# Kernel tuning notes

Measured on AMD Instinct MI355X. Metric: run time of the kernel, lower is better.

The kernel has to match this reference:

```python
import jax, jax.numpy as jnp
import numpy as np

B, P, ENC, DEC, EMB, ATT, V, L = 32, 196, 2048, 512, 512, 512, 32000, 21
T = L - 1  # decode steps


def setup_inputs() -> dict:
    key = jax.random.key(0)
    ks = jax.random.split(key, 20)
    u = lambda k, s, a=0.1: jax.random.uniform(k, s, jnp.float32, -a, a)
    lens = jax.random.randint(ks[1], (B, 1), 5, L + 1)
    lens = lens.at[0, 0].set(L)  # force max_decode_len == T (static)
    return {
        'encoder_out': jax.random.normal(ks[0], (B, P, ENC), jnp.float32),
        'encoded_captions': jax.random.randint(ks[2], (B, L), 0, V),
        'caption_lengths': lens,
        'emb_W': u(ks[3], (V, EMB)),
        'W_ea': u(ks[4], (ATT, ENC), 0.02), 'b_ea': jnp.zeros((ATT,)),
        'W_da': u(ks[5], (ATT, DEC), 0.02), 'b_da': jnp.zeros((ATT,)),
        'w_fa': u(ks[6], (1, ATT), 0.02), 'b_fa': jnp.zeros((1,)),
        'W_ih': u(ks[7], (4 * DEC, EMB + ENC), 0.02), 'b_ih': jnp.zeros((4 * DEC,)),
        'W_hh': u(ks[8], (4 * DEC, DEC), 0.02), 'b_hh': jnp.zeros((4 * DEC,)),
        'W_h0': u(ks[9], (DEC, ENC), 0.02), 'b_h0': jnp.zeros((DEC,)),
        'W_c0': u(ks[10], (DEC, ENC), 0.02), 'b_c0': jnp.zeros((DEC,)),
        'W_fb': u(ks[11], (ENC, DEC), 0.02), 'b_fb': jnp.zeros((ENC,)),
        'W_fc': u(ks[12], (V, DEC)), 'b_fc': jnp.zeros((V,)),
    }


def reference(encoder_out, encoded_captions, caption_lengths, emb_W,
              W_ea, b_ea, W_da, b_da, w_fa, b_fa,
              W_ih, b_ih, W_hh, b_hh, W_h0, b_h0, W_c0, b_c0,
              W_fb, b_fb, W_fc, b_fc):
    # sort by caption length descending (as in torch forward)
    lens = caption_lengths[:, 0]
    sort_ind = jnp.argsort(-lens)
    lens_s = lens[sort_ind]
    enc = encoder_out[sort_ind]          # [B,P,ENC]
    caps = encoded_captions[sort_ind]    # [B,L]
    dec_lens = lens_s - 1

    mean_enc = enc.mean(axis=1)
    h0 = mean_enc @ W_h0.T + b_h0
    c0 = mean_enc @ W_c0.T + b_c0

    att1 = jnp.einsum('bpe,ae->bpa', enc, W_ea) + b_ea  # precompute encoder attn proj
    embs = emb_W[caps]                                   # [B,L,EMB]
    emb_seq = jnp.transpose(embs[:, :T], (1, 0, 2))      # [T,B,EMB] (teacher forcing)
    mask_seq = jnp.arange(T)[:, None] < dec_lens[None, :]  # [T,B]

    def step(carry, xs):
        h, c = carry
        emb_t, m = xs  # [B,EMB], [B] bool; m emulates shrinking batch_size_t
        att2 = h @ W_da.T + b_da
        e = jnp.maximum(att1 + att2[:, None, :], 0.0) @ w_fa[0] + b_fa[0]  # [B,P]
        alpha = jax.nn.softmax(e, axis=1)
        awe = jnp.einsum('bp,bpe->be', alpha, enc)
        gate = jax.nn.sigmoid(h @ W_fb.T + b_fb)
        x = jnp.concatenate([emb_t, gate * awe], axis=1)
        g = x @ W_ih.T + b_ih + h @ W_hh.T + b_hh
        i, f, gg, o = jnp.split(g, 4, axis=1)
        c_new = jax.nn.sigmoid(f) * c + jax.nn.sigmoid(i) * jnp.tanh(gg)
        h_new = jax.nn.sigmoid(o) * jnp.tanh(c_new)
        preds = h_new @ W_fc.T + b_fc  # dropout in eval mode (identity)
        mf = m[:, None]
        h = jnp.where(mf, h_new, h)
        c = jnp.where(mf, c_new, c)
        preds = preds * mf.astype(preds.dtype)
        alpha = alpha * mf.astype(alpha.dtype)
        return (h, c), (preds, alpha)

    _, (preds, alphas) = jax.lax.scan(step, (h0, c0), (emb_seq, mask_seq))
    predictions = jnp.transpose(preds, (1, 0, 2))  # [B,T,V]
    alphas = jnp.transpose(alphas, (1, 0, 2))      # [B,T,P]
    return predictions, alphas
```

## Files before the change

### kernel.cpp

```cpp
#include <hip/hip_runtime.h>
#include <hip/hip_bf16.h>
#include <cstddef>

#define NB 32
#define NP 196
#define NE 2048
#define ND 512
#define NV 32000
#define NL 21
#define NT 20

typedef __attribute__((ext_vector_type(8))) short short8;
typedef __attribute__((ext_vector_type(4))) float f32x4;

__device__ __forceinline__ unsigned short f2b(float f) {
    __hip_bfloat16 h = __float2bfloat16(f);
    return *reinterpret_cast<unsigned short*>(&h);
}
__device__ __forceinline__ float b2f(unsigned short u) {
    union { unsigned int i; float f; } v; v.i = (unsigned)u << 16; return v.f;
}
__device__ __forceinline__ float b2f_lo(unsigned int u) {
    union { unsigned int i; float f; } v; v.i = u << 16; return v.f;
}
__device__ __forceinline__ float b2f_hi(unsigned int u) {
    union { unsigned int i; float f; } v; v.i = u & 0xffff0000u; return v.f;
}


__global__ void k_sort(const int* __restrict__ lens, int* __restrict__ sind, int* __restrict__ dlens,
                       int* __restrict__ rowmap, int* __restrict__ mpad)
{
    int i = threadIdx.x;
    if (i < NB) {
        int li = lens[i];
        int r = 0;
        for (int j = 0; j < NB; ++j) {
            int lj = lens[j];
            if (lj > li || (lj == li && j < i)) ++r;
        }
        sind[r] = i;
        dlens[r] = li - 1;
    }
    __syncthreads();
    if (i == 0) {
        int c = 0;
        for (int t = 0; t < NT; ++t)
            for (int b = 0; b < NB; ++b)
                if (t < dlens[b]) rowmap[c++] = t * NB + b;
        int pad = (c + 63) & ~63;
        for (int r = c; r < pad; ++r) rowmap[r] = -1;
        mpad[0] = pad;
    }
}

__global__ __launch_bounds__(256) void k_conv_enc(
    const float* __restrict__ enc, const int* __restrict__ sind,
    unsigned short* __restrict__ encB)
{
    int idx = (blockIdx.x * 256 + threadIdx.x) * 8;
    int b = idx / (NP * NE), rem = idx - b * (NP * NE);
    const float* src = enc + (size_t)sind[b] * NP * NE + rem;
    float4 a = *reinterpret_cast<const float4*>(src);
    float4 c = *reinterpret_cast<const float4*>(src + 4);
    uint4 o;
    o.x = f2b(a.x) | ((unsigned)f2b(a.y) << 16);
    o.y = f2b(a.z) | ((unsigned)f2b(a.w) << 16);
    o.z = f2b(c.x) | ((unsigned)f2b(c.y) << 16);
    o.w = f2b(c.z) | ((unsigned)f2b(c.w) << 16);
    *reinterpret_cast<uint4*>(encB + idx) = o;
}

__global__ __launch_bounds__(256) void k_mean(const float* __restrict__ enc, const int* __restrict__ sind,
                                              float* __restrict__ mean_enc)
{
    int b = blockIdx.y;
    int k = blockIdx.x * 256 + threadIdx.x;
    const float* e = enc + (size_t)sind[b] * NP * NE + k;
    float s0 = 0.f, s1 = 0.f, s2 = 0.f, s3 = 0.f;
    for (int p = 0; p < NP; p += 4) {
        s0 += e[(size_t)(p + 0) * NE];
        s1 += e[(size_t)(p + 1) * NE];
        s2 += e[(size_t)(p + 2) * NE];
        s3 += e[(size_t)(p + 3) * NE];
    }
    mean_enc[(size_t)b * NE + k] = (s0 + s1 + s2 + s3) * (1.0f / NP);
}

__global__ __launch_bounds__(256) void k_zero(const int* __restrict__ dlens, float* __restrict__ out)
{
    int b = blockIdx.x / NT, t = blockIdx.x % NT;
    if (t < dlens[b]) return;
    float4 z = {0.f, 0.f, 0.f, 0.f};
    float4* row = (float4*)(out + ((size_t)b * NT + t) * NV);
    for (int i = threadIdx.x; i < NV / 4; i += 256) row[i] = z;
}

__global__ __launch_bounds__(256) void gemm_skinny_split(
    const float* __restrict__ A0, const float* __restrict__ W0a, const float* __restrict__ W0b,
    float* __restrict__ spart)
{
    __shared__ float As[32][32];
    __shared__ float Ws[64][33];
    int n0 = blockIdx.x * 64;
    int ks = blockIdx.y;
    int tid = threadIdx.x;
    int lb = tid / 8, lkq = tid % 8;
    int b4 = (tid / 32) * 4, nl = (tid % 32) * 2;
    float acc[4][2] = {};
    for (int kt = ks * 256; kt < ks * 256 + 256; kt += 32) {
        float4 a4 = *reinterpret_cast<const float4*>(A0 + (size_t)lb * NE + kt + lkq * 4);
        As[lkq * 4 + 0][lb] = a4.x; As[lkq * 4 + 1][lb] = a4.y;
        As[lkq * 4 + 2][lb] = a4.z; As[lkq * 4 + 3][lb] = a4.w;
        #pragma unroll
        for (int r = 0; r < 2; ++r) {
            int s = tid + r * 256;
            int n_l = s / 8, kq = s % 8;
            int ng = n0 + n_l;
            const float* wrow = (ng < 512) ? (W0a + (size_t)ng * NE)
                                           : (W0b + (size_t)(ng - 512) * NE);
            float4 w4 = *reinterpret_cast<const float4*>(wrow + kt + kq * 4);
            Ws[n_l][kq * 4 + 0] = w4.x; Ws[n_l][kq * 4 + 1] = w4.y;
            Ws[n_l][kq * 4 + 2] = w4.z; Ws[n_l][kq * 4 + 3] = w4.w;
        }
        __syncthreads();
        #pragma unroll
        for (int k = 0; k < 32; ++k) {
            float4 av = *reinterpret_cast<const float4*>(&As[k][b4]);
            float w0 = Ws[nl][k], w1 = Ws[nl + 1][k];
            acc[0][0] += av.x * w0; acc[0][1] += av.x * w1;
            acc[1][0] += av.y * w0; acc[1][1] += av.y * w1;
            acc[2][0] += av.z * w0; acc[2][1] += av.z * w1;
            acc[3][0] += av.w * w0; acc[3][1] += av.w * w1;
        }
        __syncthreads();
    }
    float* Cp = spart + (size_t)ks * NB * 1024;
    #pragma unroll
    for (int j = 0; j < 2; ++j)
        #pragma unroll
        for (int i = 0; i < 4; ++i)
            Cp[(size_t)(b4 + i) * 1024 + n0 + nl + j] = acc[i][j];
}

__global__ __launch_bounds__(256) void k_hc0(
    const float* __restrict__ spart, const float* __restrict__ ba, const float* __restrict__ bb,
    float* __restrict__ hc, float* __restrict__ xh)
{
    int b = blockIdx.x;
    for (int ng = threadIdx.x; ng < 1024; ng += 256) {
        float s = (ng < 512) ? ba[ng] : bb[ng - 512];
        #pragma unroll
        for (int ks = 0; ks < 8; ++ks)
            s += spart[(size_t)ks * NB * 1024 + (size_t)b * 1024 + ng];
        hc[(size_t)b * 1024 + ng] = s;
        if (ng < 512) xh[(size_t)b * 3072 + 2560 + ng] = s;
    }
}

__global__ __launch_bounds__(256) void gemm_att1_mfma(
    const unsigned short* __restrict__ encB, const float* __restrict__ W_ea,
    const float* __restrict__ bias, unsigned short* __restrict__ att1B)
{
    int fid = blockIdx.x;
    int c = fid & 7, x = (fid >> 3) & 7, pg = fid >> 6;
    int p = pg * 8 + c;
    if (p >= 98) return;
    int bm0 = p * 64, bn0 = x * 64;
    __shared__ unsigned short As[64][40];
    __shared__ unsigned short Bs[64][40];
    int tid = threadIdx.x;
    int w = tid >> 6, lane = tid & 63;
    int srow = tid >> 2, schunk = (tid & 3) * 8;
    const unsigned short* arow = encB + (size_t)(bm0 + srow) * NE + schunk;
    const float* brow = W_ea + (size_t)(bn0 + srow) * NE + schunk;
    int frow = lane & 15, fk = (lane >> 4) * 8;
    f32x4 acc[4] = {};
    for (int kt = 0; kt < NE; kt += 32) {
        uint4 av = *reinterpret_cast<const uint4*>(arow + kt);
        float4 b0 = *reinterpret_cast<const float4*>(brow + kt);
        float4 b1 = *reinterpret_cast<const float4*>(brow + kt + 4);
        uint4 bv;
        bv.x = f2b(b0.x) | ((unsigned)f2b(b0.y) << 16);
        bv.y = f2b(b0.z) | ((unsigned)f2b(b0.w) << 16);
        bv.z = f2b(b1.x) | ((unsigned)f2b(b1.y) << 16);
        bv.w = f2b(b1.z) | ((unsigned)f2b(b1.w) << 16);
        *reinterpret_cast<uint4*>(&As[srow][schunk]) = av;
        *reinterpret_cast<uint4*>(&Bs[srow][schunk]) = bv;
        __syncthreads();
        short8 af = *reinterpret_cast<const short8*>(&As[w * 16 + frow][fk]);
        #pragma unroll
        for (int n = 0; n < 4; ++n) {
            short8 bf = *reinterpret_cast<const short8*>(&Bs[n * 16 + frow][fk]);
            acc[n] = __builtin_amdgcn_mfma_f32_16x16x32_bf16(af, bf, acc[n], 0, 0, 0);
        }
        __syncthreads();
    }
    int crow = bm0 + w * 16 + (lane >> 4) * 4;
    int ccol0 = lane & 15;
    #pragma unroll
    for (int n = 0; n < 4; ++n) {
        int col = bn0 + n * 16 + ccol0;
        float bb2 = bias[col];
        #pragma unroll
        for (int i = 0; i < 4; ++i)
            att1B[(size_t)(crow + i) * ND + col] = f2b(acc[n][i] + bb2);
    }
}

__global__ __launch_bounds__(256) void gemm_preds_mfma(
    const unsigned short* __restrict__ hseqB, const float* __restrict__ W_fc,
    const float* __restrict__ bias, float* __restrict__ out,
    const int* __restrict__ rowmap, const int* __restrict__ mpad)
{
    int fid = blockIdx.x;
    int c = fid & 7;
    int rem = fid >> 3;
    int m = rem % 10, g = rem / 10;
    int n = g * 8 + c;
    if (n >= 250) return;
    int bm0 = m * 64;
    if (bm0 >= mpad[0]) return;
    int bn0 = n * 128;
    __shared__ unsigned short As[64][40];
    __shared__ unsigned short Bs[128][40];
    int tid = threadIdx.x;
    int w = tid >> 6, lane = tid & 63;
    int srow = tid >> 2, schunk = (tid & 3) * 8;
    int rid = rowmap[bm0 + srow];
    const unsigned short* aptr = hseqB + (size_t)(rid < 0 ? 0 : rid) * ND + schunk;
    const float* bptr0 = W_fc + (size_t)(bn0 + srow) * ND + schunk;
    const float* bptr1 = W_fc + (size_t)(bn0 + 64 + srow) * ND + schunk;
    int frow = lane & 15, fk = (lane >> 4) * 8;
    f32x4 acc[8] = {};
    for (int kt = 0; kt < ND; kt += 32) {
        uint4 av = *reinterpret_cast<const uint4*>(aptr + kt);
        float4 c0 = *reinterpret_cast<const float4*>(bptr0 + kt);
        float4 c1 = *reinterpret_cast<const float4*>(bptr0 + kt + 4);
        float4 d0 = *reinterpret_cast<const float4*>(bptr1 + kt);
        float4 d1 = *reinterpret_cast<const float4*>(bptr1 + kt + 4);
        uint4 bv0, bv1;
        bv0.x = f2b(c0.x) | ((unsigned)f2b(c0.y) << 16);
        bv0.y = f2b(c0.z) | ((unsigned)f2b(c0.w) << 16);
        bv0.z = f2b(c1.x) | ((unsigned)f2b(c1.y) << 16);
        bv0.w = f2b(c1.z) | ((unsigned)f2b(c1.w) << 16);
        bv1.x = f2b(d0.x) | ((unsigned)f2b(d0.y) << 16);
        bv1.y = f2b(d0.z) | ((unsigned)f2b(d0.w) << 16);
        bv1.z = f2b(d1.x) | ((unsigned)f2b(d1.y) << 16);
        bv1.w = f2b(d1.z) | ((unsigned)f2b(d1.w) << 16);
        *reinterpret_cast<uint4*>(&As[srow][schunk]) = av;
        *reinterpret_cast<uint4*>(&Bs[srow][schunk]) = bv0;
        *reinterpret_cast<uint4*>(&Bs[64 + srow][schunk]) = bv1;
        __syncthreads();
        short8 af = *reinterpret_cast<const short8*>(&As[w * 16 + frow][fk]);
        #pragma unroll
        for (int nn = 0; nn < 8; ++nn) {
            short8 bf = *reinterpret_cast<const short8*>(&Bs[nn * 16 + frow][fk]);
            acc[nn] = __builtin_amdgcn_mfma_f32_16x16x32_bf16(af, bf, acc[nn], 0, 0, 0);
        }
        __syncthreads();
    }
    int rl0 = w * 16 + (lane >> 4) * 4;
    int ccol0 = lane & 15;
    #pragma unroll
    for (int i = 0; i < 4; ++i) {
        int rm = rowmap[bm0 + rl0 + i];
        if (rm < 0) continue;
        int t = rm / NB, b = rm % NB;
        float* orow = out + ((size_t)b * NT + t) * NV;
        #pragma unroll
        for (int nn = 0; nn < 8; ++nn) {
            int col = bn0 + nn * 16 + ccol0;
            orow[col] = acc[nn][i] + bias[col];
        }
    }
}

__global__ __launch_bounds__(256) void k_attg(
    const float* __restrict__ hc, const float* __restrict__ W_da, const float* __restrict__ W_fb,
    const float* __restrict__ b_da, const float* __restrict__ b_fb, float* __restrict__ attg)
{
    __shared__ float As[32][32];
    __shared__ float Ws[64][33];
    int n0 = blockIdx.x * 64;
    int tid = threadIdx.x;
    int lb = tid / 8, lkq = tid % 8;
    int b4 = (tid / 32) * 4, nl = (tid % 32) * 2;
    float acc[4][2] = {};
    for (int kt = 0; kt < 512; kt += 32) {
        float4 a4 = *reinterpret_cast<const float4*>(hc + (size_t)lb * 1024 + kt + lkq * 4);
        As[lkq * 4 + 0][lb] = a4.x; As[lkq * 4 + 1][lb] = a4.y;
        As[lkq * 4 + 2][lb] = a4.z; As[lkq * 4 + 3][lb] = a4.w;
        #pragma unroll
        for (int r = 0; r < 2; ++r) {
            int s = tid + r * 256;
            int n_l = s / 8, kq = s % 8;
            int ng = n0 + n_l;
            const float* wrow = (ng < 512) ? (W_da + (size_t)ng * 512)
                                           : (W_fb + (size_t)(ng - 512) * 512);
            float4 w4 = *reinterpret_cast<const float4*>(wrow + kt + kq * 4);
            Ws[n_l][kq * 4 + 0] = w4.x; Ws[n_l][kq * 4 + 1] = w4.y;
            Ws[n_l][kq * 4 + 2] = w4.z; Ws[n_l][kq * 4 + 3] = w4.w;
        }
        __syncthreads();
        #pragma unroll
        for (int k = 0; k < 32; ++k) {
            float4 av = *reinterpret_cast<const float4*>(&As[k][b4]);
            float w0 = Ws[nl][k], w1 = Ws[nl + 1][k];
            acc[0][0] += av.x * w0; acc[0][1] += av.x * w1;
            acc[1][0] += av.y * w0; acc[1][1] += av.y * w1;
            acc[2][0] += av.z * w0; acc[2][1] += av.z * w1;
            acc[3][0] += av.w * w0; acc[3][1] += av.w * w1;
        }
        __syncthreads();
    }
    #pragma unroll
    for (int j = 0; j < 2; ++j) {
        int ng = n0 + nl + j;
        float bias = (ng < 512) ? b_da[ng] : b_fb[ng - 512];
        #pragma unroll
        for (int i = 0; i < 4; ++i)
            attg[(size_t)(b4 + i) * 2560 + ng] = acc[i][j] + bias;
    }
}

__global__ __launch_bounds__(256) void k_e(
    const unsigned short* __restrict__ att1B, const float* __restrict__ attg,
    const float* __restrict__ w_fa, const float* __restrict__ b_fa,
    float* __restrict__ e)
{
    __shared__ float att2s[ND];
    __shared__ float wfas[ND];
    int b = blockIdx.y, tid = threadIdx.x;
    const float* ag = attg + (size_t)b * 2560;
    for (int d = tid; d < ND; d += 256) { att2s[d] = ag[d]; wfas[d] = w_fa[d]; }
    __syncthreads();
    int w = tid >> 6, lane = tid & 63;
    int p0 = blockIdx.x * 28;
    const unsigned short* a1 = att1B + ((size_t)b * NP + p0) * ND;
    #pragma unroll
    for (int i = 0; i < 7; ++i) {
        int p = w + 4 * i;
        const unsigned short* row = a1 + (size_t)p * ND;
        float s = 0.f;
        #pragma unroll
        for (int j = 0; j < 2; ++j) {
            int d = j * 256 + lane * 4;
            uint2 u = *reinterpret_cast<const uint2*>(row + d);
            float v0 = b2f_lo(u.x), v1 = b2f_hi(u.x);
            float v2 = b2f_lo(u.y), v3 = b2f_hi(u.y);
            float4 a2 = *reinterpret_cast<const float4*>(&att2s[d]);
            float4 wf = *reinterpret_cast<const float4*>(&wfas[d]);
            s += fmaxf(v0 + a2.x, 0.f) * wf.x + fmaxf(v1 + a2.y, 0.f) * wf.y
               + fmaxf(v2 + a2.z, 0.f) * wf.z + fmaxf(v3 + a2.w, 0.f) * wf.w;
        }
        for (int off = 32; off > 0; off >>= 1) s += __shfl_down(s, off);
        if (lane == 0) e[(size_t)b * NP + p0 + p] = s + b_fa[0];
    }
}

__global__ __launch_bounds__(256) void k_awe(
    const unsigned short* __restrict__ encB, const int* __restrict__ dlens,
    const int* __restrict__ sind, const int* __restrict__ caps, const float* __restrict__ emb_W,
    const float* __restrict__ e, const float* __restrict__ attg,
    float* __restrict__ xh, float* __restrict__ out_alpha, int t)
{
    __shared__ float es[256];
    __shared__ float red[256];
    int kc = blockIdx.x, b = blockIdx.y, tid = threadIdx.x;
    float ev = -1e30f;
    if (tid < NP) { float v = e[(size_t)b * NP + tid]; es[tid] = v; ev = v; }
    red[tid] = ev; __syncthreads();
    for (int s2 = 128; s2 > 0; s2 >>= 1) { if (tid < s2) red[tid] = fmaxf(red[tid], red[tid + s2]); __syncthreads(); }
    float m = red[0]; __syncthreads();
    float xe = (tid < NP) ? expf(es[tid] - m) : 0.f;
    red[tid] = xe; __syncthreads();
    for (int s2 = 128; s2 > 0; s2 >>= 1) { if (tid < s2) red[tid] += red[tid + s2]; __syncthreads(); }
    float inv = 1.0f / red[0];
    __syncthreads();
    es[tid] = xe * inv;
    __syncthreads();

    int k = kc * 256 + tid;
    const unsigned short* ec = encB + (size_t)b * NP * NE + k;
    float s0 = 0.f, s1 = 0.f, s2v = 0.f, s3 = 0.f;
    #pragma unroll 4
    for (int p = 0; p < NP; p += 4) {
        s0 += es[p + 0] * b2f(ec[(size_t)(p + 0) * NE]);
        s1 += es[p + 1] * b2f(ec[(size_t)(p + 1) * NE]);
        s2v += es[p + 2] * b2f(ec[(size_t)(p + 2) * NE]);
        s3 += es[p + 3] * b2f(ec[(size_t)(p + 3) * NE]);
    }
    float awe = (s0 + s1) + (s2v + s3);
    float gp = attg[(size_t)b * 2560 + 512 + k];
    float gate = 1.f / (1.f + expf(-gp));
    xh[(size_t)b * 3072 + 512 + k] = gate * awe;
    if (kc == 0) {
        bool live = (t < dlens[b]);
        if (tid < NP) out_alpha[((size_t)b * NT + t) * NP + tid] = live ? es[tid] : 0.f;
        const float* er = emb_W + (size_t)caps[sind[b] * NL + t] * ND;
        xh[(size_t)b * 3072 + tid] = er[tid];
        xh[(size_t)b * 3072 + 256 + tid] = er[256 + tid];
    }
}

__global__ __launch_bounds__(256) void k_gates(
    const float* __restrict__ xh, const float* __restrict__ W_ih, const float* __restrict__ W_hh,
    float* __restrict__ gpart)
{
    __shared__ float smem[3200];
    int blk = blockIdx.x, tid = threadIdx.x;
    int nt = blk & 31, ks = blk >> 5;
    float* As = smem;
    float (*Ws)[33] = (float(*)[33])(smem + 1024);
    int n0 = nt * 64;
    int lb = tid / 8, lkq = tid % 8;
    int b4 = (tid / 32) * 4, nl = (tid % 32) * 2;
    float acc[4][2] = {};
    for (int kt = ks * 768; kt < ks * 768 + 768; kt += 32) {
        float4 a4 = *reinterpret_cast<const float4*>(xh + (size_t)lb * 3072 + kt + lkq * 4);
        As[(lkq * 4 + 0) * 32 + lb] = a4.x; As[(lkq * 4 + 1) * 32 + lb] = a4.y;
        As[(lkq * 4 + 2) * 32 + lb] = a4.z; As[(lkq * 4 + 3) * 32 + lb] = a4.w;
        #pragma unroll
        for (int r = 0; r < 2; ++r) {
            int s = tid + r * 256;
            int n_l = s / 8, kq = s % 8;
            int ng = n0 + n_l;
            int kk = kt + kq * 4;
            const float* wrow = (kk < 2560) ? (W_ih + (size_t)ng * 2560 + kk)
                                            : (W_hh + (size_t)ng * 512 + (kk - 2560));
            float4 w4 = *reinterpret_cast<const float4*>(wrow);
            Ws[n_l][kq * 4 + 0] = w4.x; Ws[n_l][kq * 4 + 1] = w4.y;
            Ws[n_l][kq * 4 + 2] = w4.z; Ws[n_l][kq * 4 + 3] = w4.w;
        }
        __syncthreads();
        #pragma unroll
        for (int k = 0; k < 32; ++k) {
            float4 av = *reinterpret_cast<const float4*>(&As[k * 32 + b4]);
            float w0 = Ws[nl][k], w1 = Ws[nl + 1][k];
            acc[0][0] += av.x * w0; acc[0][1] += av.x * w1;
            acc[1][0] += av.y * w0; acc[1][1] += av.y * w1;
            acc[2][0] += av.z * w0; acc[2][1] += av.z * w1;
            acc[3][0] += av.w * w0; acc[3][1] += av.w * w1;
        }
        __syncthreads();
    }
    float* Cp = gpart + (size_t)ks * NB * 2048;
    #pragma unroll
    for (int j = 0; j < 2; ++j)
        #pragma unroll
        for (int i = 0; i < 4; ++i)
            Cp[(size_t)(b4 + i) * 2048 + n0 + nl + j] = acc[i][j];
}

__global__ __launch_bounds__(256) void k_cell(
    const float* __restrict__ gpart, const int* __restrict__ dlens,
    const float* __restrict__ b_ih, const float* __restrict__ b_hh,
    float* __restrict__ hc, unsigned short* __restrict__ hseqB, float* __restrict__ xh, int t)
{
    int b = blockIdx.x;
    for (int d = threadIdx.x; d < ND; d += 256) {
        float g0 = b_ih[d] + b_hh[d];
        float g1 = b_ih[512 + d] + b_hh[512 + d];
        float g2 = b_ih[1024 + d] + b_hh[1024 + d];
        float g3 = b_ih[1536 + d] + b_hh[1536 + d];
        #pragma unroll
        for (int ks = 0; ks < 4; ++ks) {
            const float* gp = gpart + ((size_t)ks * NB + b) * 2048;
            g0 += gp[d]; g1 += gp[512 + d]; g2 += gp[1024 + d]; g3 += gp[1536 + d];
        }
        float ig = 1.f / (1.f + expf(-g0));
        float fg = 1.f / (1.f + expf(-g1));
        float gt = tanhf(g2);
        float og = 1.f / (1.f + expf(-g3));
        float c_old = hc[(size_t)b * 1024 + 512 + d];
        float c_new = fg * c_old + ig * gt;
        float h_new = og * tanhf(c_new);
        hseqB[((size_t)t * NB + b) * ND + d] = f2b(h_new);
        if (t < dlens[b]) {
            hc[(size_t)b * 1024 + d] = h_new;
            hc[(size_t)b * 1024 + 512 + d] = c_new;
            xh[(size_t)b * 3072 + 2560 + d] = h_new;
        }
    }
}

extern "C" void kernel_launch(void* const* d_in, const int* in_sizes, int n_in,
                              void* d_out, int out_size, void* d_ws, size_t ws_size,
                              hipStream_t stream)
{
    const float* enc   = (const float*)d_in[0];
    const int*   caps  = (const int*)d_in[1];
    const int*   clens = (const int*)d_in[2];
    const float* emb_W = (const float*)d_in[3];
    const float* W_ea  = (const float*)d_in[4];
    const float* b_ea  = (const float*)d_in[5];
    const float* W_da  = (const float*)d_in[6];
    const float* b_da  = (const float*)d_in[7];
    const float* w_fa  = (const float*)d_in[8];
    const float* b_fa  = (const float*)d_in[9];
    const float* W_ih  = (const float*)d_in[10];
    const float* b_ih  = (const float*)d_in[11];
    const float* W_hh  = (const float*)d_in[12];
    const float* b_hh  = (const float*)d_in[13];
    const float* W_h0  = (const float*)d_in[14];
    const float* b_h0  = (const float*)d_in[15];
    const float* W_c0  = (const float*)d_in[16];
    const float* b_c0  = (const float*)d_in[17];
    const float* W_fb  = (const float*)d_in[18];
    const float* b_fb  = (const float*)d_in[19];
    const float* W_fc  = (const float*)d_in[20];
    const float* b_fc  = (const float*)d_in[21];

    float* out = (float*)d_out;
    float* out_alpha = out + (size_t)NB * NT * NV;

    int* iws    = (int*)d_ws;
    int* sind   = iws;
    int* dlens  = iws + 32;
    int* rowmap = iws + 64;
    int* mpad   = iws + 704;
    float* base = (float*)d_ws + 1024;
    float* mean_enc = base;
    float* hc    = mean_enc + NB * NE;
    float* attg  = hc + NB * 1024;
    float* xh    = attg + NB * 2560;
    float* e     = xh + NB * 3072;
    float* gpart = e + NB * NP;
    unsigned short* att1B = (unsigned short*)(gpart + 262144);
    unsigned short* hseqB = att1B + (size_t)NB * NP * ND;
    unsigned short* encB  = hseqB + (size_t)NT * NB * ND;

    k_sort<<<1, 64, 0, stream>>>(clens, sind, dlens, rowmap, mpad);
    k_zero<<<NB * NT, 256, 0, stream>>>(dlens, out);
    k_conv_enc<<<dim3(NB * NP * NE / 2048), 256, 0, stream>>>(enc, sind, encB);
    k_mean<<<dim3(NE / 256, NB), 256, 0, stream>>>(enc, sind, mean_enc);
    gemm_skinny_split<<<dim3(16, 8), 256, 0, stream>>>(mean_enc, W_h0, W_c0, gpart);
    k_hc0<<<dim3(NB), 256, 0, stream>>>(gpart, b_h0, b_c0, hc, xh);
    gemm_att1_mfma<<<dim3(832), 256, 0, stream>>>(encB, W_ea, b_ea, att1B);

    for (int t = 0; t < NT; ++t) {
        k_attg<<<dim3(40), 256, 0, stream>>>(hc, W_da, W_fb, b_da, b_fb, attg);
        k_e<<<dim3(7, NB), 256, 0, stream>>>(att1B, attg, w_fa, b_fa, e);
        k_awe<<<dim3(8, NB), 256, 0, stream>>>(encB, dlens, sind, caps, emb_W,
                                               e, attg, xh, out_alpha, t);
        k_gates<<<dim3(128), 256, 0, stream>>>(xh, W_ih, W_hh, gpart);
        k_cell<<<dim3(NB), 256, 0, stream>>>(gpart, dlens, b_ih, b_hh, hc, hseqB, xh, t);
    }

    gemm_preds_mfma<<<dim3(2560), 256, 0, stream>>>(hseqB, W_fc, b_fc, out, rowmap, mpad);
}
```

Before: 1.805 ms.

## Move embedding and recurrent gate GEMMs off the attention critical path

The embedding and W_hh parts of the LSTM gate GEMM are now computed in the first phase of each step, alongside the attention/gate projection, since they do not depend on the attention output. The post-attention gate kernel then only covers the 2048-wide attention-weighted encoding slice, which shortens the serial chain per step. Embeddings are gathered for all steps up front by a new kernel. The att1 GEMM now reads and converts fp32 encoder rows directly instead of the bf16 copy. The cell kernel sums six partial buffers instead of four.

Result: faster. 1.580 ms (median of 2 runs) (-12.5%).

```diff
diff --git a/kernel.cpp b/kernel.cpp
--- a/kernel.cpp
+++ b/kernel.cpp
@@ -71,6 +71,17 @@
     *reinterpret_cast<uint4*>(encB + idx) = o;
 }
 
+__global__ __launch_bounds__(256) void k_emb(
+    const int* __restrict__ caps, const int* __restrict__ sind,
+    const float* __restrict__ emb_W, float* __restrict__ embS)
+{
+    int t = blockIdx.x, b = blockIdx.y;
+    const float* src = emb_W + (size_t)caps[sind[b] * NL + t] * ND;
+    float* dst = embS + ((size_t)t * NB + b) * ND;
+    int i = threadIdx.x * 2;
+    *reinterpret_cast<float2*>(dst + i) = *reinterpret_cast<const float2*>(src + i);
+}
+
 __global__ __launch_bounds__(256) void k_mean(const float* __restrict__ enc, const int* __restrict__ sind,
                                               float* __restrict__ mean_enc)
 {
@@ -96,11 +107,44 @@
     for (int i = threadIdx.x; i < NV / 4; i += 256) row[i] = z;
 }
 
+__device__ __forceinline__ void tile_body_uniW(
+    const float* __restrict__ A, int lda, const float* __restrict__ W, int wstride,
+    int n0, int kbeg, int kend, float* As, float (*Ws)[33], float acc[4][2],
+    int tid)
+{
+    int lb = tid / 8, lkq = tid % 8;
+    int b4 = (tid / 32) * 4, nl = (tid % 32) * 2;
+    for (int kt = kbeg; kt < kend; kt += 32) {
+        float4 a4 = *reinterpret_cast<const float4*>(A + (size_t)lb * lda + kt + lkq * 4);
+        As[(lkq * 4 + 0) * 32 + lb] = a4.x; As[(lkq * 4 + 1) * 32 + lb] = a4.y;
+        As[(lkq * 4 + 2) * 32 + lb] = a4.z; As[(lkq * 4 + 3) * 32 + lb] = a4.w;
+        #pragma unroll
+        for (int r = 0; r < 2; ++r) {
+            int s = tid + r * 256;
+            int n_l = s / 8, kq = s % 8;
+            float4 w4 = *reinterpret_cast<const float4*>(W + (size_t)(n0 + n_l) * wstride + kt + kq * 4);
+            Ws[n_l][kq * 4 + 0] = w4.x; Ws[n_l][kq * 4 + 1] = w4.y;
+            Ws[n_l][kq * 4 + 2] = w4.z; Ws[n_l][kq * 4 + 3] = w4.w;
+        }
+        __syncthreads();
+        #pragma unroll
+        for (int k = 0; k < 32; ++k) {
+            float4 av = *reinterpret_cast<const float4*>(&As[k * 32 + b4]);
+            float w0 = Ws[nl][k], w1 = Ws[nl + 1][k];
+            acc[0][0] += av.x * w0; acc[0][1] += av.x * w1;
+            acc[1][0] += av.y * w0; acc[1][1] += av.y * w1;
+            acc[2][0] += av.z * w0; acc[2][1] += av.z * w1;
+            acc[3][0] += av.w * w0; acc[3][1] += av.w * w1;
+        }
+        __syncthreads();
+    }
+}
+
 __global__ __launch_bounds__(256) void gemm_skinny_split(
     const float* __restrict__ A0, const float* __restrict__ W0a, const float* __restrict__ W0b,
     float* __restrict__ spart)
 {
-    __shared__ float As[32][32];
+    __shared__ float As[1024];
     __shared__ float Ws[64][33];
     int n0 = blockIdx.x * 64;
     int ks = blockIdx.y;
@@ -110,8 +154,8 @@
     float acc[4][2] = {};
     for (int kt = ks * 256; kt < ks * 256 + 256; kt += 32) {
         float4 a4 = *reinterpret_cast<const float4*>(A0 + (size_t)lb * NE + kt + lkq * 4);
-        As[lkq * 4 + 0][lb] = a4.x; As[lkq * 4 + 1][lb] = a4.y;
-        As[lkq * 4 + 2][lb] = a4.z; As[lkq * 4 + 3][lb] = a4.w;
+        As[(lkq * 4 + 0) * 32 + lb] = a4.x; As[(lkq * 4 + 1) * 32 + lb] = a4.y;
+        As[(lkq * 4 + 2) * 32 + lb] = a4.z; As[(lkq * 4 + 3) * 32 + lb] = a4.w;
         #pragma unroll
         for (int r = 0; r < 2; ++r) {
             int s = tid + r * 256;
@@ -126,7 +170,7 @@
         __syncthreads();
         #pragma unroll
         for (int k = 0; k < 32; ++k) {
-            float4 av = *reinterpret_cast<const float4*>(&As[k][b4]);
+            float4 av = *reinterpret_cast<const float4*>(&As[k * 32 + b4]);
             float w0 = Ws[nl][k], w1 = Ws[nl + 1][k];
             acc[0][0] += av.x * w0; acc[0][1] += av.x * w1;
             acc[1][0] += av.y * w0; acc[1][1] += av.y * w1;
@@ -145,7 +189,7 @@
 
 __global__ __launch_bounds__(256) void k_hc0(
     const float* __restrict__ spart, const float* __restrict__ ba, const float* __restrict__ bb,
-    float* __restrict__ hc, float* __restrict__ xh)
+    float* __restrict__ hc)
 {
     int b = blockIdx.x;
     for (int ng = threadIdx.x; ng < 1024; ng += 256) {
@@ -154,13 +198,13 @@
         for (int ks = 0; ks < 8; ++ks)
             s += spart[(size_t)ks * NB * 1024 + (size_t)b * 1024 + ng];
         hc[(size_t)b * 1024 + ng] = s;
-        if (ng < 512) xh[(size_t)b * 3072 + 2560 + ng] = s;
     }
 }
 
 __global__ __launch_bounds__(256) void gemm_att1_mfma(
-    const unsigned short* __restrict__ encB, const float* __restrict__ W_ea,
-    const float* __restrict__ bias, unsigned short* __restrict__ att1B)
+    const float* __restrict__ enc, const float* __restrict__ W_ea,
+    const float* __restrict__ bias, unsigned short* __restrict__ att1B,
+    const int* __restrict__ sind)
 {
     int fid = blockIdx.x;
     int c = fid & 7, x = (fid >> 3) & 7, pg = fid >> 6;
@@ -172,15 +216,22 @@
     int tid = threadIdx.x;
     int w = tid >> 6, lane = tid & 63;
     int srow = tid >> 2, schunk = (tid & 3) * 8;
-    const unsigned short* arow = encB + (size_t)(bm0 + srow) * NE + schunk;
+    int mg = bm0 + srow;
+    int bidx = mg / NP, pp = mg - bidx * NP;
+    const float* arow = enc + ((size_t)sind[bidx] * NP + pp) * NE + schunk;
     const float* brow = W_ea + (size_t)(bn0 + srow) * NE + schunk;
     int frow = lane & 15, fk = (lane >> 4) * 8;
     f32x4 acc[4] = {};
     for (int kt = 0; kt < NE; kt += 32) {
-        uint4 av = *reinterpret_cast<const uint4*>(arow + kt);
+        float4 a0 = *reinterpret_cast<const float4*>(arow + kt);
+        float4 a1 = *reinterpret_cast<const float4*>(arow + kt + 4);
         float4 b0 = *reinterpret_cast<const float4*>(brow + kt);
         float4 b1 = *reinterpret_cast<const float4*>(brow + kt + 4);
-        uint4 bv;
+        uint4 av, bv;
+        av.x = f2b(a0.x) | ((unsigned)f2b(a0.y) << 16);
+        av.y = f2b(a0.z) | ((unsigned)f2b(a0.w) << 16);
+        av.z = f2b(a1.x) | ((unsigned)f2b(a1.y) << 16);
+        av.w = f2b(a1.z) | ((unsigned)f2b(a1.w) << 16);
         bv.x = f2b(b0.x) | ((unsigned)f2b(b0.y) << 16);
         bv.y = f2b(b0.z) | ((unsigned)f2b(b0.w) << 16);
         bv.z = f2b(b1.x) | ((unsigned)f2b(b1.y) << 16);
@@ -276,51 +327,73 @@
     }
 }
 
-__global__ __launch_bounds__(256) void k_attg(
+__global__ __launch_bounds__(256) void k_phase1(
     const float* __restrict__ hc, const float* __restrict__ W_da, const float* __restrict__ W_fb,
-    const float* __restrict__ b_da, const float* __restrict__ b_fb, float* __restrict__ attg)
-{
-    __shared__ float As[32][32];
+    const float* __restrict__ b_da, const float* __restrict__ b_fb,
+    const float* __restrict__ embS, const float* __restrict__ W_ih, const float* __restrict__ W_hh,
+    float* __restrict__ attg, float* __restrict__ gpart, int t)
+{
+    __shared__ float As[1024];
     __shared__ float Ws[64][33];
-    int n0 = blockIdx.x * 64;
-    int tid = threadIdx.x;
-    int lb = tid / 8, lkq = tid % 8;
+    int blk = blockIdx.x, tid = threadIdx.x;
     int b4 = (tid / 32) * 4, nl = (tid % 32) * 2;
     float acc[4][2] = {};
-    for (int kt = 0; kt < 512; kt += 32) {
-        float4 a4 = *reinterpret_cast<const float4*>(hc + (size_t)lb * 1024 + kt + lkq * 4);
-        As[lkq * 4 + 0][lb] = a4.x; As[lkq * 4 + 1][lb] = a4.y;
-        As[lkq * 4 + 2][lb] = a4.z; As[lkq * 4 + 3][lb] = a4.w;
-        #pragma unroll
-        for (int r = 0; r < 2; ++r) {
-            int s = tid + r * 256;
-            int n_l = s / 8, kq = s % 8;
-            int ng = n0 + n_l;
-            const float* wrow = (ng < 512) ? (W_da + (size_t)ng * 512)
-                                           : (W_fb + (size_t)(ng - 512) * 512);
-            float4 w4 = *reinterpret_cast<const float4*>(wrow + kt + kq * 4);
-            Ws[n_l][kq * 4 + 0] = w4.x; Ws[n_l][kq * 4 + 1] = w4.y;
-            Ws[n_l][kq * 4 + 2] = w4.z; Ws[n_l][kq * 4 + 3] = w4.w;
-        }
-        __syncthreads();
-        #pragma unroll
-        for (int k = 0; k < 32; ++k) {
-            float4 av = *reinterpret_cast<const float4*>(&As[k][b4]);
-            float w0 = Ws[nl][k], w1 = Ws[nl + 1][k];
-            acc[0][0] += av.x * w0; acc[0][1] += av.x * w1;
-            acc[1][0] += av.y * w0; acc[1][1] += av.y * w1;
-            acc[2][0] += av.z * w0; acc[2][1] += av.z * w1;
-            acc[3][0] += av.w * w0; acc[3][1] += av.w * w1;
-        }
-        __syncthreads();
-    }
-    #pragma unroll
-    for (int j = 0; j < 2; ++j) {
-        int ng = n0 + nl + j;
-        float bias = (ng < 512) ? b_da[ng] : b_fb[ng - 512];
-        #pragma unroll
-        for (int i = 0; i < 4; ++i)
-            attg[(size_t)(b4 + i) * 2560 + ng] = acc[i][j] + bias;
+    if (blk < 40) {
+        int n0 = blk * 64;
+        int lb = tid / 8, lkq = tid % 8;
+        for (int kt = 0; kt < 512; kt += 32) {
+            float4 a4 = *reinterpret_cast<const float4*>(hc + (size_t)lb * 1024 + kt + lkq * 4);
+            As[(lkq * 4 + 0) * 32 + lb] = a4.x; As[(lkq * 4 + 1) * 32 + lb] = a4.y;
+            As[(lkq * 4 + 2) * 32 + lb] = a4.z; As[(lkq * 4 + 3) * 32 + lb] = a4.w;
+            #pragma unroll
+            for (int r = 0; r < 2; ++r) {
+                int s = tid + r * 256;
+                int n_l = s / 8, kq = s % 8;
+                int ng = n0 + n_l;
+                const float* wrow = (ng < 512) ? (W_da + (size_t)ng * 512)
+                                               : (W_fb + (size_t)(ng - 512) * 512);
+                float4 w4 = *reinterpret_cast<const float4*>(wrow + kt + kq * 4);
+                Ws[n_l][kq * 4 + 0] = w4.x; Ws[n_l][kq * 4 + 1] = w4.y;
+                Ws[n_l][kq * 4 + 2] = w4.z; Ws[n_l][kq * 4 + 3] = w4.w;
+            }
+            __syncthreads();
+            #pragma unroll
+            for (int k = 0; k < 32; ++k) {
+                float4 av = *reinterpret_cast<const float4*>(&As[k * 32 + b4]);
+                float w0 = Ws[nl][k], w1 = Ws[nl + 1][k];
+                acc[0][0] += av.x * w0; acc[0][1] += av.x * w1;
+                acc[1][0] += av.y * w0; acc[1][1] += av.y * w1;
+                acc[2][0] += av.z * w0; acc[2][1] += av.z * w1;
+                acc[3][0] += av.w * w0; acc[3][1] += av.w * w1;
+            }
+            __syncthreads();
+        }
+        #pragma unroll
+        for (int j = 0; j < 2; ++j) {
+            int ng = n0 + nl + j;
+            float bias = (ng < 512) ? b_da[ng] : b_fb[ng - 512];
+            #pragma unroll
+            for (int i = 0; i < 4; ++i)
+                attg[(size_t)(b4 + i) * 2560 + ng] = acc[i][j] + bias;
+        }
+    } else if (blk < 72) {
+        int nt = blk - 40, n0 = nt * 64;
+        tile_body_uniW(embS + (size_t)t * NB * ND, ND, W_ih, 2560, n0, 0, 512, As, Ws, acc, tid);
+        float* Cp = gpart + (size_t)4 * NB * 2048;
+        #pragma unroll
+        for (int j = 0; j < 2; ++j)
+            #pragma unroll
+            for (int i = 0; i < 4; ++i)
+                Cp[(size_t)(b4 + i) * 2048 + n0 + nl + j] = acc[i][j];
+    } else {
+        int nt = blk - 72, n0 = nt * 64;
+        tile_body_uniW(hc, 1024, W_hh, 512, n0, 0, 512, As, Ws, acc, tid);
+        float* Cp = gpart + (size_t)5 * NB * 2048;
+        #pragma unroll
+        for (int j = 0; j < 2; ++j)
+            #pragma unroll
+            for (int i = 0; i < 4; ++i)
+                Cp[(size_t)(b4 + i) * 2048 + n0 + nl + j] = acc[i][j];
     }
 }
 
@@ -361,7 +434,6 @@
 
 __global__ __launch_bounds__(256) void k_awe(
     const unsigned short* __restrict__ encB, const int* __restrict__ dlens,
-    const int* __restrict__ sind, const int* __restrict__ caps, const float* __restrict__ emb_W,
     const float* __restrict__ e, const float* __restrict__ attg,
     float* __restrict__ xh, float* __restrict__ out_alpha, int t)
 {
@@ -395,56 +467,25 @@
     float gp = attg[(size_t)b * 2560 + 512 + k];
     float gate = 1.f / (1.f + expf(-gp));
     xh[(size_t)b * 3072 + 512 + k] = gate * awe;
-    if (kc == 0) {
+    if (kc == 0 && tid < NP) {
         bool live = (t < dlens[b]);
-        if (tid < NP) out_alpha[((size_t)b * NT + t) * NP + tid] = live ? es[tid] : 0.f;
-        const float* er = emb_W + (size_t)caps[sind[b] * NL + t] * ND;
-        xh[(size_t)b * 3072 + tid] = er[tid];
-        xh[(size_t)b * 3072 + 256 + tid] = er[256 + tid];
+        out_alpha[((size_t)b * NT + t) * NP + tid] = live ? es[tid] : 0.f;
     }
 }
 
 __global__ __launch_bounds__(256) void k_gates(
-    const float* __restrict__ xh, const float* __restrict__ W_ih, const float* __restrict__ W_hh,
+    const float* __restrict__ xh, const float* __restrict__ W_ih,
     float* __restrict__ gpart)
 {
-    __shared__ float smem[3200];
+    __shared__ float As[1024];
+    __shared__ float Ws[64][33];
     int blk = blockIdx.x, tid = threadIdx.x;
     int nt = blk & 31, ks = blk >> 5;
-    float* As = smem;
-    float (*Ws)[33] = (float(*)[33])(smem + 1024);
     int n0 = nt * 64;
-    int lb = tid / 8, lkq = tid % 8;
     int b4 = (tid / 32) * 4, nl = (tid % 32) * 2;
     float acc[4][2] = {};
-    for (int kt = ks * 768; kt < ks * 768 + 768; kt += 32) {
-        float4 a4 = *reinterpret_cast<const float4*>(xh + (size_t)lb * 3072 + kt + lkq * 4);
-        As[(lkq * 4 + 0) * 32 + lb] = a4.x; As[(lkq * 4 + 1) * 32 + lb] = a4.y;
-        As[(lkq * 4 + 2) * 32 + lb] = a4.z; As[(lkq * 4 + 3) * 32 + lb] = a4.w;
-        #pragma unroll
-        for (int r = 0; r < 2; ++r) {
-            int s = tid + r * 256;
-            int n_l = s / 8, kq = s % 8;
-            int ng = n0 + n_l;
-            int kk = kt + kq * 4;
-            const float* wrow = (kk < 2560) ? (W_ih + (size_t)ng * 2560 + kk)
-                                            : (W_hh + (size_t)ng * 512 + (kk - 2560));
-            float4 w4 = *reinterpret_cast<const float4*>(wrow);
-            Ws[n_l][kq * 4 + 0] = w4.x; Ws[n_l][kq * 4 + 1] = w4.y;
-            Ws[n_l][kq * 4 + 2] = w4.z; Ws[n_l][kq * 4 + 3] = w4.w;
-        }
-        __syncthreads();
-        #pragma unroll
-        for (int k = 0; k < 32; ++k) {
-            float4 av = *reinterpret_cast<const float4*>(&As[k * 32 + b4]);
-            float w0 = Ws[nl][k], w1 = Ws[nl + 1][k];
-            acc[0][0] += av.x * w0; acc[0][1] += av.x * w1;
-            acc[1][0] += av.y * w0; acc[1][1] += av.y * w1;
-            acc[2][0] += av.z * w0; acc[2][1] += av.z * w1;
-            acc[3][0] += av.w * w0; acc[3][1] += av.w * w1;
-        }
-        __syncthreads();
-    }
+    tile_body_uniW(xh + 512 + (size_t)ks * 512, 3072, W_ih + 512 + (size_t)ks * 512, 2560,
+                   n0, 0, 512, As, Ws, acc, tid);
     float* Cp = gpart + (size_t)ks * NB * 2048;
     #pragma unroll
     for (int j = 0; j < 2; ++j)
@@ -456,7 +497,7 @@
 __global__ __launch_bounds__(256) void k_cell(
     const float* __restrict__ gpart, const int* __restrict__ dlens,
     const float* __restrict__ b_ih, const float* __restrict__ b_hh,
-    float* __restrict__ hc, unsigned short* __restrict__ hseqB, float* __restrict__ xh, int t)
+    float* __restrict__ hc, unsigned short* __restrict__ hseqB, int t)
 {
     int b = blockIdx.x;
     for (int d = threadIdx.x; d < ND; d += 256) {
@@ -465,7 +506,7 @@
         float g2 = b_ih[1024 + d] + b_hh[1024 + d];
         float g3 = b_ih[1536 + d] + b_hh[1536 + d];
         #pragma unroll
-        for (int ks = 0; ks < 4; ++ks) {
+        for (int ks = 0; ks < 6; ++ks) {
             const float* gp = gpart + ((size_t)ks * NB + b) * 2048;
             g0 += gp[d]; g1 += gp[512 + d]; g2 += gp[1024 + d]; g3 += gp[1536 + d];
         }
@@ -480,7 +521,6 @@
         if (t < dlens[b]) {
             hc[(size_t)b * 1024 + d] = h_new;
             hc[(size_t)b * 1024 + 512 + d] = c_new;
-            xh[(size_t)b * 3072 + 2560 + d] = h_new;
         }
     }
 }
@@ -526,26 +566,28 @@
     float* attg  = hc + NB * 1024;
     float* xh    = attg + NB * 2560;
     float* e     = xh + NB * 3072;
-    float* gpart = e + NB * NP;
-    unsigned short* att1B = (unsigned short*)(gpart + 262144);
+    float* embS  = e + NB * NP;
+    float* gpart = embS + (size_t)NT * NB * ND;
+    unsigned short* att1B = (unsigned short*)(gpart + 6 * NB * 2048);
     unsigned short* hseqB = att1B + (size_t)NB * NP * ND;
     unsigned short* encB  = hseqB + (size_t)NT * NB * ND;
 
     k_sort<<<1, 64, 0, stream>>>(clens, sind, dlens, rowmap, mpad);
     k_zero<<<NB * NT, 256, 0, stream>>>(dlens, out);
     k_conv_enc<<<dim3(NB * NP * NE / 2048), 256, 0, stream>>>(enc, sind, encB);
+    k_emb<<<dim3(NT, NB), 256, 0, stream>>>(caps, sind, emb_W, embS);
     k_mean<<<dim3(NE / 256, NB), 256, 0, stream>>>(enc, sind, mean_enc);
     gemm_skinny_split<<<dim3(16, 8), 256, 0, stream>>>(mean_enc, W_h0, W_c0, gpart);
-    k_hc0<<<dim3(NB), 256, 0, stream>>>(gpart, b_h0, b_c0, hc, xh);
-    gemm_att1_mfma<<<dim3(832), 256, 0, stream>>>(encB, W_ea, b_ea, att1B);
+    k_hc0<<<dim3(NB), 256, 0, stream>>>(gpart, b_h0, b_c0, hc);
+    gemm_att1_mfma<<<dim3(832), 256, 0, stream>>>(enc, W_ea, b_ea, att1B, sind);
 
     for (int t = 0; t < NT; ++t) {
-        k_attg<<<dim3(40), 256, 0, stream>>>(hc, W_da, W_fb, b_da, b_fb, attg);
+        k_phase1<<<dim3(104), 256, 0, stream>>>(hc, W_da, W_fb, b_da, b_fb,
+                                                embS, W_ih, W_hh, attg, gpart, t);
         k_e<<<dim3(7, NB), 256, 0, stream>>>(att1B, attg, w_fa, b_fa, e);
-        k_awe<<<dim3(8, NB), 256, 0, stream>>>(encB, dlens, sind, caps, emb_W,
-                                               e, attg, xh, out_alpha, t);
-        k_gates<<<dim3(128), 256, 0, stream>>>(xh, W_ih, W_hh, gpart);
-        k_cell<<<dim3(NB), 256, 0, stream>>>(gpart, dlens, b_ih, b_hh, hc, hseqB, xh, t);
+        k_awe<<<dim3(8, NB), 256, 0, stream>>>(encB, dlens, e, attg, xh, out_alpha, t);
+        k_gates<<<dim3(128), 256, 0, stream>>>(xh, W_ih, gpart);
+        k_cell<<<dim3(NB), 256, 0, stream>>>(gpart, dlens, b_ih, b_hh, hc, hseqB, t);
     }
 
     gemm_preds_mfma<<<dim3(2560), 256, 0, stream>>>(hseqB, W_fc, b_fc, out, rowmap, mpad);
```
